# Performance work log

Hardware: AMD Instinct MI355X
Metric: run time of the kernel (lower is better)

The kernel has to match this reference:

```python
import jax, jax.numpy as jnp
import numpy as np

jax.config.update("jax_enable_x64", True)

P = 2013265921          # NTT-friendly prime 15 * 2**27 + 1 (int64-safe proxy for BLS12-377 Fr)
GEN = 31                # generator of the multiplicative group of F_P
LOGN = 22
N = 1 << LOGN           # domain_size
C = 4                   # columns, as in the module docstring example


def _pow_table(base, n):
    """powers[k] = base**k mod P for k in [0, n), built by repeated doubling (vectorized)."""
    pw = np.ones(n, dtype=np.int64)
    cur = base % P
    step = 1
    while step < n:
        hi = min(2 * step, n)
        pw[step:hi] = (pw[:hi - step] * cur) % P
        cur = (cur * cur) % P
        step *= 2
    return pw


def setup_inputs() -> dict:
    key = jax.random.key(0)
    x = jax.random.randint(key, (N, C), 0, P, dtype=jnp.int64)
    omega = pow(GEN, (P - 1) // N, P)          # primitive N-th root of unity
    omega_inv = pow(omega, P - 2, P)           # its inverse (Fermat)
    twiddles = jnp.asarray(_pow_table(omega_inv, N // 2))  # omega_inv**k, k < N/2  (the 'Params' table)
    n_inv = jnp.asarray(pow(N, P - 2, P), dtype=jnp.int64)  # N^{-1} mod P
    return {"input": x, "twiddles": twiddles, "n_inv": n_inv}


def reference(input, twiddles, n_inv):
    """Inverse NTT over F_P, columns transformed independently. Output in natural order."""
    n, c = input.shape
    logn = n.bit_length() - 1
    # bit-reversal permutation indices (static; computed with numpy)
    idx = np.arange(n)
    rev = np.zeros(n, dtype=np.int64)
    for i in range(logn):
        rev = (rev << 1) | ((idx >> i) & 1)
    x = input[rev]
    # iterative Cooley-Tukey butterflies, logn stages
    for s in range(1, logn + 1):
        m = 1 << s
        half = m >> 1
        w = twiddles[:: n // m]                 # [half] = omega_inv**(j * n/m)
        xr = x.reshape(-1, m, c)                # [n/m, m, c]
        lo, hi = xr[:, :half], xr[:, half:]
        t = (w[None, :, None] * hi) % P         # modular twiddle multiply
        x = jnp.concatenate([(lo + t) % P, (lo - t) % P], axis=1).reshape(n, c)
    return (x * n_inv) % P                      # scale by N^{-1}
```

## Files before the change

### kernel.cpp

```cpp
#include <hip/hip_runtime.h>
#include <stdint.h>

static constexpr uint32_t P = 2013265921u;
static constexpr int      LOGM = 11;
static constexpr int      MSZ  = 1 << LOGM;
static constexpr int      NCOL = 2;

__host__ __device__ constexpr uint32_t neg_pinv32() {
    uint32_t x = 1u;
    for (int i = 0; i < 5; ++i) x *= 2u - P * x;
    return 0u - x;
}
static constexpr uint32_t NEG_PINV = neg_pinv32();
static constexpr uint32_t R1 = (uint32_t)(((uint64_t)1 << 32) % P);
static constexpr uint32_t R2 = (uint32_t)(((uint64_t)R1 * R1) % P);

__device__ __forceinline__ uint32_t mont_mul(uint32_t a, uint32_t b) {
    uint32_t tlo = a * b;
    uint32_t thi = __umulhi(a, b);
    uint32_t m   = tlo * NEG_PINV;
    uint32_t r   = thi + __umulhi(m, P) + (tlo != 0u);
    uint32_t s   = r - P;
    return s < r ? s : r;
}
__device__ __forceinline__ uint32_t to_mont(uint32_t a) { return mont_mul(a, R2); }

__device__ __forceinline__ uint32_t shoup_mul(uint32_t w, uint32_t wp, uint32_t x) {
    uint32_t q = __umulhi(wp, x);
    uint32_t t = w * x - q * P;
    uint32_t s = t - P;
    return s < t ? s : t;
}
__device__ __forceinline__ uint32_t add_p(uint32_t a, uint32_t b) {
    uint32_t r = a + b, s = r - P; return s < r ? s : r;
}
__device__ __forceinline__ uint32_t sub_p(uint32_t a, uint32_t b) {
    uint32_t r = a - b, s = r + P; return s < r ? s : r;
}
__device__ __forceinline__ uint4 mm4(uint32_t w, uint4 v) {
    return make_uint4(mont_mul(w, v.x), mont_mul(w, v.y),
                      mont_mul(w, v.z), mont_mul(w, v.w));
}
__device__ __forceinline__ void bf4_sh(uint4& L, uint4& H, uint2 w) {
    uint4 t = make_uint4(shoup_mul(w.x, w.y, H.x), shoup_mul(w.x, w.y, H.y),
                         shoup_mul(w.x, w.y, H.z), shoup_mul(w.x, w.y, H.w));
    uint4 l = L;
    L = make_uint4(add_p(l.x, t.x), add_p(l.y, t.y), add_p(l.z, t.z), add_p(l.w, t.w));
    H = make_uint4(sub_p(l.x, t.x), sub_p(l.y, t.y), sub_p(l.z, t.z), sub_p(l.w, t.w));
}
__device__ __forceinline__ void bf4_mont(uint4& L, uint4& H, uint32_t wm) {
    uint4 t = mm4(wm, H);
    uint4 l = L;
    L = make_uint4(add_p(l.x, t.x), add_p(l.y, t.y), add_p(l.z, t.z), add_p(l.w, t.w));
    H = make_uint4(sub_p(l.x, t.x), sub_p(l.y, t.y), sub_p(l.z, t.z), sub_p(l.w, t.w));
}
__device__ __forceinline__ void bf4_triv(uint4& L, uint4& H) {
    uint4 l = L, h = H;
    L = make_uint4(add_p(l.x, h.x), add_p(l.y, h.y), add_p(l.z, h.z), add_p(l.w, h.w));
    H = make_uint4(sub_p(l.x, h.x), sub_p(l.y, h.y), sub_p(l.z, h.z), sub_p(l.w, h.w));
}

__device__ __forceinline__ int g_sw(int el) {
    return el ^ (((el >> 3) ^ (el >> 6)) & 7);
}
__device__ __forceinline__ int fidx(int el, int c4) { return (g_sw(el) << 1) | c4; }

__device__ __forceinline__ void radix8_sh(uint4 x[8],
        uint2 ta, uint2 tb0, uint2 tb1,
        uint2 tc0, uint2 tc1, uint2 tc2, uint2 tc3) {
    bf4_sh(x[0], x[1], ta);  bf4_sh(x[2], x[3], ta);
    bf4_sh(x[4], x[5], ta);  bf4_sh(x[6], x[7], ta);
    bf4_sh(x[0], x[2], tb0); bf4_sh(x[1], x[3], tb1);
    bf4_sh(x[4], x[6], tb0); bf4_sh(x[5], x[7], tb1);
    bf4_sh(x[0], x[4], tc0); bf4_sh(x[1], x[5], tc1);
    bf4_sh(x[2], x[6], tc2); bf4_sh(x[3], x[7], tc3);
}

template <bool PASS2>
__global__ __launch_bounds__(512, 4) void intt_pass(
        const uint4* __restrict__ src, uint4* __restrict__ dst,
        const uint32_t* __restrict__ tw,
        const uint32_t* __restrict__ ninv_p)
{
    __shared__ uint4 buf[MSZ * NCOL];
    __shared__ uint2 stab[2047];

    const int      t   = threadIdx.x;
    const int      c4  = t & 1;
    const int      sub = t >> 1;
    const uint32_t bid = blockIdx.x;
    const uint32_t grp = ((bid & 7u) << 7) | (bid >> 3);
    const uint32_t c   = (grp << 1) | (uint32_t)c4;

    uint32_t wv[4]; int ev[4];
#pragma unroll
    for (int q = 0; q < 4; ++q) {
        int e = t + (q << 9);
        ev[q] = e;
        if (e < 2047) {
            uint32_t ep1 = (uint32_t)e + 1u;
            int sm1 = 31 - __clz((int)ep1);
            uint32_t j = ep1 - (1u << sm1);
            wv[q] = tw[j << (21 - sm1)];
        }
    }

    const uint32_t r8 = __brev((uint32_t)sub) >> 24;
    uint4 x[8];
#pragma unroll
    for (int m = 0; m < 8; ++m) {
        uint32_t r3 = __brev((uint32_t)m) >> 29;
        x[m] = src[((r3 << 8) | r8) * (uint32_t)MSZ + c];
    }

#pragma unroll
    for (int q = 0; q < 4; ++q) {
        if (ev[q] < 2047) {
            uint32_t w  = wv[q];
            uint32_t wp = (uint32_t)((((uint64_t)w) << 32) / P);
            stab[ev[q]] = make_uint2(w, wp);
        }
    }

    const uint32_t u1 = to_mont(tw[1u << 20]);
    const uint32_t u2 = to_mont(tw[1u << 19]);
    const uint32_t u3 = to_mont(tw[3u << 19]);

    bf4_triv(x[0], x[1]);  bf4_triv(x[2], x[3]);
    bf4_triv(x[4], x[5]);  bf4_triv(x[6], x[7]);
    bf4_triv(x[0], x[2]);  bf4_mont(x[1], x[3], u1);
    bf4_triv(x[4], x[6]);  bf4_mont(x[5], x[7], u1);
    bf4_triv(x[0], x[4]);  bf4_mont(x[1], x[5], u2);
    bf4_mont(x[2], x[6], u1); bf4_mont(x[3], x[7], u3);
#pragma unroll
    for (int m = 0; m < 8; ++m) buf[fidx(8 * sub + m, c4)] = x[m];
    __syncthreads();

    {
        const int L = sub & 7, hi = sub >> 3;
        const int base = (hi << 6) | L;
#pragma unroll
        for (int m = 0; m < 8; ++m) x[m] = buf[fidx(base | (m << 3), c4)];
        radix8_sh(x, stab[7 + L], stab[15 + L], stab[23 + L],
                     stab[31 + L], stab[39 + L], stab[47 + L], stab[55 + L]);
#pragma unroll
        for (int m = 0; m < 8; ++m) buf[fidx(base | (m << 3), c4)] = x[m];
    }
    __syncthreads();

    {
        const int L = sub & 63, hi = sub >> 6;
        const int base = (hi << 9) | L;
#pragma unroll
        for (int m = 0; m < 8; ++m) x[m] = buf[fidx(base | (m << 6), c4)];
        radix8_sh(x, stab[63 + L], stab[127 + L], stab[191 + L],
                     stab[255 + L], stab[319 + L], stab[383 + L], stab[447 + L]);
#pragma unroll
        for (int m = 0; m < 8; ++m) buf[fidx(base | (m << 6), c4)] = x[m];
    }
    __syncthreads();

    uint32_t nm = 0u, s256 = 0u, step512 = 0u, tm0 = 0u;
    if (PASS2) {
        nm = to_mont(*ninv_p);
    } else {
        s256    = to_mont(tw[c << 8]);
        step512 = mont_mul(s256, s256);
        tm0     = to_mont(tw[c * (uint32_t)sub]);
    }
#pragma unroll
    for (int gg = 0; gg < 2; ++gg) {
        const int lo = sub + (gg << 8);
        uint4 y[4];
#pragma unroll
        for (int m = 0; m < 4; ++m) y[m] = buf[fidx(lo | (m << 9), c4)];
        const uint2 t10  = stab[511 + lo];
        const uint2 t110 = stab[1023 + lo];
        const uint2 t111 = stab[1535 + lo];
        bf4_sh(y[0], y[1], t10);  bf4_sh(y[2], y[3], t10);
        bf4_sh(y[0], y[2], t110); bf4_sh(y[1], y[3], t111);

        if (!PASS2) {
            uint32_t tm = tm0;
#pragma unroll
            for (int m = 0; m < 4; ++m) {
                dst[c * (uint32_t)MSZ + (uint32_t)((m << 9) | lo)] = mm4(tm, y[m]);
                tm = mont_mul(tm, step512);
            }
            tm0 = mont_mul(tm0, s256);
        } else {
#pragma unroll
            for (int m = 0; m < 4; ++m)
                dst[(uint32_t)((m << 9) | lo) * (uint32_t)MSZ + c] = mm4(nm, y[m]);
        }
    }
}

extern "C" void kernel_launch(void* const* d_in, const int* in_sizes, int n_in,
                              void* d_out, int out_size, void* d_ws, size_t ws_size,
                              hipStream_t stream)
{
    const uint4*    x    = (const uint4*)d_in[0];
    const uint32_t* tw   = (const uint32_t*)d_in[1];
    const uint32_t* ninv = (const uint32_t*)d_in[2];
    uint4*          out  = (uint4*)d_out;

    intt_pass<false><<<dim3(1024), dim3(512), 0, stream>>>(x, out, tw, ninv);
    intt_pass<true ><<<dim3(1024), dim3(512), 0, stream>>>(out, out, tw, ninv);
}
```

Before: 193.0 us.

## Process two column groups per block with prefetch and shrink twiddle table

Each block now handles two column groups in sequence, halving the grid. While the first group finishes its final stages, the block prefetches the second group's inputs into registers. The Shoup twiddle table is cut from 2047 to 511 entries. The last two stages instead take their twiddles from a 512-entry Montgomery table and derive the remaining ones with extra multiplies. This reduces per-block setup cost (twiddle loads and 64-bit divisions) and overlaps global loads with compute, at the cost of more registers, fewer blocks and extra Montgomery multiplies.

```diff
diff --git a/kernel.cpp b/kernel.cpp
--- a/kernel.cpp
+++ b/kernel.cpp
@@ -82,116 +82,129 @@
         const uint32_t* __restrict__ tw,
         const uint32_t* __restrict__ ninv_p)
 {
-    __shared__ uint4 buf[MSZ * NCOL];
-    __shared__ uint2 stab[2047];
+    __shared__ uint4    buf[MSZ * NCOL];
+    __shared__ uint2    stab[511];
+    __shared__ uint32_t mtab[512];
 
     const int      t   = threadIdx.x;
     const int      c4  = t & 1;
     const int      sub = t >> 1;
     const uint32_t bid = blockIdx.x;
-    const uint32_t grp = ((bid & 7u) << 7) | (bid >> 3);
-    const uint32_t c   = (grp << 1) | (uint32_t)c4;
-
-    uint32_t wv[4]; int ev[4];
-#pragma unroll
-    for (int q = 0; q < 4; ++q) {
-        int e = t + (q << 9);
-        ev[q] = e;
-        if (e < 2047) {
-            uint32_t ep1 = (uint32_t)e + 1u;
-            int sm1 = 31 - __clz((int)ep1);
-            uint32_t j = ep1 - (1u << sm1);
-            wv[q] = tw[j << (21 - sm1)];
-        }
-    }
+    const uint32_t grp = ((bid & 7u) << 6) | (bid >> 3);
+    const uint32_t c0  = (grp << 1) | (uint32_t)c4;
+
+    uint32_t wv = 0u;
+    if (t < 511) {
+        uint32_t ep1 = (uint32_t)t + 1u;
+        int sm1 = 31 - __clz((int)ep1);
+        uint32_t j = ep1 - (1u << sm1);
+        wv = tw[j << (21 - sm1)];
+    }
+    uint32_t mv = tw[(uint32_t)t << 11];
 
     const uint32_t r8 = __brev((uint32_t)sub) >> 24;
     uint4 x[8];
 #pragma unroll
     for (int m = 0; m < 8; ++m) {
         uint32_t r3 = __brev((uint32_t)m) >> 29;
-        x[m] = src[((r3 << 8) | r8) * (uint32_t)MSZ + c];
-    }
-
-#pragma unroll
-    for (int q = 0; q < 4; ++q) {
-        if (ev[q] < 2047) {
-            uint32_t w  = wv[q];
-            uint32_t wp = (uint32_t)((((uint64_t)w) << 32) / P);
-            stab[ev[q]] = make_uint2(w, wp);
-        }
-    }
+        x[m] = src[((r3 << 8) | r8) * (uint32_t)MSZ + c0];
+    }
+
+    if (t < 511) {
+        uint32_t wp = (uint32_t)((((uint64_t)wv) << 32) / P);
+        stab[t] = make_uint2(wv, wp);
+    }
+    mtab[t] = to_mont(mv);
 
     const uint32_t u1 = to_mont(tw[1u << 20]);
     const uint32_t u2 = to_mont(tw[1u << 19]);
     const uint32_t u3 = to_mont(tw[3u << 19]);
-
-    bf4_triv(x[0], x[1]);  bf4_triv(x[2], x[3]);
-    bf4_triv(x[4], x[5]);  bf4_triv(x[6], x[7]);
-    bf4_triv(x[0], x[2]);  bf4_mont(x[1], x[3], u1);
-    bf4_triv(x[4], x[6]);  bf4_mont(x[5], x[7], u1);
-    bf4_triv(x[0], x[4]);  bf4_mont(x[1], x[5], u2);
-    bf4_mont(x[2], x[6], u1); bf4_mont(x[3], x[7], u3);
-#pragma unroll
-    for (int m = 0; m < 8; ++m) buf[fidx(8 * sub + m, c4)] = x[m];
-    __syncthreads();
-
-    {
-        const int L = sub & 7, hi = sub >> 3;
-        const int base = (hi << 6) | L;
-#pragma unroll
-        for (int m = 0; m < 8; ++m) x[m] = buf[fidx(base | (m << 3), c4)];
-        radix8_sh(x, stab[7 + L], stab[15 + L], stab[23 + L],
-                     stab[31 + L], stab[39 + L], stab[47 + L], stab[55 + L]);
-#pragma unroll
-        for (int m = 0; m < 8; ++m) buf[fidx(base | (m << 3), c4)] = x[m];
-    }
-    __syncthreads();
-
-    {
-        const int L = sub & 63, hi = sub >> 6;
-        const int base = (hi << 9) | L;
-#pragma unroll
-        for (int m = 0; m < 8; ++m) x[m] = buf[fidx(base | (m << 6), c4)];
-        radix8_sh(x, stab[63 + L], stab[127 + L], stab[191 + L],
-                     stab[255 + L], stab[319 + L], stab[383 + L], stab[447 + L]);
-#pragma unroll
-        for (int m = 0; m < 8; ++m) buf[fidx(base | (m << 6), c4)] = x[m];
-    }
-    __syncthreads();
-
-    uint32_t nm = 0u, s256 = 0u, step512 = 0u, tm0 = 0u;
-    if (PASS2) {
-        nm = to_mont(*ninv_p);
-    } else {
-        s256    = to_mont(tw[c << 8]);
-        step512 = mont_mul(s256, s256);
-        tm0     = to_mont(tw[c * (uint32_t)sub]);
-    }
-#pragma unroll
-    for (int gg = 0; gg < 2; ++gg) {
-        const int lo = sub + (gg << 8);
-        uint4 y[4];
-#pragma unroll
-        for (int m = 0; m < 4; ++m) y[m] = buf[fidx(lo | (m << 9), c4)];
-        const uint2 t10  = stab[511 + lo];
-        const uint2 t110 = stab[1023 + lo];
-        const uint2 t111 = stab[1535 + lo];
-        bf4_sh(y[0], y[1], t10);  bf4_sh(y[2], y[3], t10);
-        bf4_sh(y[0], y[2], t110); bf4_sh(y[1], y[3], t111);
-
+    uint32_t nm = 0u;
+    if (PASS2) nm = to_mont(*ninv_p);
+
+    uint4 xn[8];
+#pragma unroll
+    for (int it = 0; it < 2; ++it) {
+        const uint32_t c = c0 + (uint32_t)(it << 10);
+        if (it) {
+            __syncthreads();
+#pragma unroll
+            for (int m = 0; m < 8; ++m) x[m] = xn[m];
+        }
+
+        bf4_triv(x[0], x[1]);  bf4_triv(x[2], x[3]);
+        bf4_triv(x[4], x[5]);  bf4_triv(x[6], x[7]);
+        bf4_triv(x[0], x[2]);  bf4_mont(x[1], x[3], u1);
+        bf4_triv(x[4], x[6]);  bf4_mont(x[5], x[7], u1);
+        bf4_triv(x[0], x[4]);  bf4_mont(x[1], x[5], u2);
+        bf4_mont(x[2], x[6], u1); bf4_mont(x[3], x[7], u3);
+#pragma unroll
+        for (int m = 0; m < 8; ++m) buf[fidx(8 * sub + m, c4)] = x[m];
+        __syncthreads();
+
+        {
+            const int L = sub & 7, hi = sub >> 3;
+            const int base = (hi << 6) | L;
+#pragma unroll
+            for (int m = 0; m < 8; ++m) x[m] = buf[fidx(base | (m << 3), c4)];
+            radix8_sh(x, stab[7 + L], stab[15 + L], stab[23 + L],
+                         stab[31 + L], stab[39 + L], stab[47 + L], stab[55 + L]);
+#pragma unroll
+            for (int m = 0; m < 8; ++m) buf[fidx(base | (m << 3), c4)] = x[m];
+        }
+        __syncthreads();
+
+        {
+            const int L = sub & 63, hi = sub >> 6;
+            const int base = (hi << 9) | L;
+#pragma unroll
+            for (int m = 0; m < 8; ++m) x[m] = buf[fidx(base | (m << 6), c4)];
+            radix8_sh(x, stab[63 + L], stab[127 + L], stab[191 + L],
+                         stab[255 + L], stab[319 + L], stab[383 + L], stab[447 + L]);
+#pragma unroll
+            for (int m = 0; m < 8; ++m) buf[fidx(base | (m << 6), c4)] = x[m];
+        }
+        __syncthreads();
+
+        if (it == 0) {
+#pragma unroll
+            for (int m = 0; m < 8; ++m) {
+                uint32_t r3 = __brev((uint32_t)m) >> 29;
+                xn[m] = src[((r3 << 8) | r8) * (uint32_t)MSZ + (c0 + 1024u)];
+            }
+        }
+
+        uint32_t s256 = 0u, step512 = 0u, tm0 = 0u;
         if (!PASS2) {
-            uint32_t tm = tm0;
-#pragma unroll
-            for (int m = 0; m < 4; ++m) {
-                dst[c * (uint32_t)MSZ + (uint32_t)((m << 9) | lo)] = mm4(tm, y[m]);
-                tm = mont_mul(tm, step512);
+            s256    = to_mont(tw[c << 8]);
+            step512 = mont_mul(s256, s256);
+            tm0     = to_mont(tw[c * (uint32_t)sub]);
+        }
+#pragma unroll
+        for (int gg = 0; gg < 2; ++gg) {
+            const int lo = sub + (gg << 8);
+            uint4 y[4];
+#pragma unroll
+            for (int m = 0; m < 4; ++m) y[m] = buf[fidx(lo | (m << 9), c4)];
+            const uint32_t M    = mtab[lo];
+            const uint32_t t10  = mont_mul(M, M);
+            const uint32_t t111 = mont_mul(M, u1);
+            bf4_mont(y[0], y[1], t10);  bf4_mont(y[2], y[3], t10);
+            bf4_mont(y[0], y[2], M);    bf4_mont(y[1], y[3], t111);
+
+            if (!PASS2) {
+                uint32_t tm = tm0;
+#pragma unroll
+                for (int m = 0; m < 4; ++m) {
+                    dst[c * (uint32_t)MSZ + (uint32_t)((m << 9) | lo)] = mm4(tm, y[m]);
+                    tm = mont_mul(tm, step512);
+                }
+                tm0 = mont_mul(tm0, s256);
+            } else {
+#pragma unroll
+                for (int m = 0; m < 4; ++m)
+                    dst[(uint32_t)((m << 9) | lo) * (uint32_t)MSZ + c] = mm4(nm, y[m]);
             }
-            tm0 = mont_mul(tm0, s256);
-        } else {
-#pragma unroll
-            for (int m = 0; m < 4; ++m)
-                dst[(uint32_t)((m << 9) | lo) * (uint32_t)MSZ + c] = mm4(nm, y[m]);
         }
     }
 }
@@ -205,6 +218,6 @@
     const uint32_t* ninv = (const uint32_t*)d_in[2];
     uint4*          out  = (uint4*)d_out;
 
-    intt_pass<false><<<dim3(1024), dim3(512), 0, stream>>>(x, out, tw, ninv);
-    intt_pass<true ><<<dim3(1024), dim3(512), 0, stream>>>(out, out, tw, ninv);
-}
+    intt_pass<false><<<dim3(512), dim3(512), 0, stream>>>(x, out, tw, ninv);
+    intt_pass<true ><<<dim3(512), dim3(512), 0, stream>>>(out, out, tw, ninv);
+}
```

New measurement: 205.4 us. +6.4%, slower.

## Restructure per-block 2048-point NTT as radix-16/16/8 with 256 threads

Applied to the files above, without the earlier changes.

Replaces the radix-8/8/8/4 decomposition over 512 threads with radix-16, radix-16, then radix-8 stages over 256 threads, each holding 16 elements in registers. This cuts the number of shared-memory round trips and barriers per pass. The shared twiddle table shrinks to 255 Shoup entries plus a 256-entry Montgomery table, and the last-stage twiddles are computed on the fly from products. The bank swizzle changes to match the new access strides. The cost is higher register pressure per thread, lower occupancy (launch bounds 256,2) and extra Montgomery multiplies in the final stage.

```diff
diff --git a/kernel.cpp b/kernel.cpp
--- a/kernel.cpp
+++ b/kernel.cpp
@@ -4,7 +4,6 @@
 static constexpr uint32_t P = 2013265921u;
 static constexpr int      LOGM = 11;
 static constexpr int      MSZ  = 1 << LOGM;
-static constexpr int      NCOL = 2;
 
 __host__ __device__ constexpr uint32_t neg_pinv32() {
     uint32_t x = 1u;
@@ -61,29 +60,19 @@
 }
 
 __device__ __forceinline__ int g_sw(int el) {
-    return el ^ (((el >> 3) ^ (el >> 6)) & 7);
+    return el ^ (((el >> 4) ^ (el >> 8)) & 3);
 }
 __device__ __forceinline__ int fidx(int el, int c4) { return (g_sw(el) << 1) | c4; }
 
-__device__ __forceinline__ void radix8_sh(uint4 x[8],
-        uint2 ta, uint2 tb0, uint2 tb1,
-        uint2 tc0, uint2 tc1, uint2 tc2, uint2 tc3) {
-    bf4_sh(x[0], x[1], ta);  bf4_sh(x[2], x[3], ta);
-    bf4_sh(x[4], x[5], ta);  bf4_sh(x[6], x[7], ta);
-    bf4_sh(x[0], x[2], tb0); bf4_sh(x[1], x[3], tb1);
-    bf4_sh(x[4], x[6], tb0); bf4_sh(x[5], x[7], tb1);
-    bf4_sh(x[0], x[4], tc0); bf4_sh(x[1], x[5], tc1);
-    bf4_sh(x[2], x[6], tc2); bf4_sh(x[3], x[7], tc3);
-}
-
 template <bool PASS2>
-__global__ __launch_bounds__(512, 4) void intt_pass(
+__global__ __launch_bounds__(256, 2) void intt_pass(
         const uint4* __restrict__ src, uint4* __restrict__ dst,
         const uint32_t* __restrict__ tw,
         const uint32_t* __restrict__ ninv_p)
 {
-    __shared__ uint4 buf[MSZ * NCOL];
-    __shared__ uint2 stab[2047];
+    __shared__ uint4    buf[MSZ * 2];
+    __shared__ uint2    stab[255];
+    __shared__ uint32_t mtab[256];
 
     const int      t   = threadIdx.x;
     const int      c4  = t & 1;
@@ -92,106 +81,135 @@
     const uint32_t grp = ((bid & 7u) << 7) | (bid >> 3);
     const uint32_t c   = (grp << 1) | (uint32_t)c4;
 
-    uint32_t wv[4]; int ev[4];
-#pragma unroll
-    for (int q = 0; q < 4; ++q) {
-        int e = t + (q << 9);
-        ev[q] = e;
-        if (e < 2047) {
-            uint32_t ep1 = (uint32_t)e + 1u;
-            int sm1 = 31 - __clz((int)ep1);
-            uint32_t j = ep1 - (1u << sm1);
-            wv[q] = tw[j << (21 - sm1)];
-        }
-    }
-
-    const uint32_t r8 = __brev((uint32_t)sub) >> 24;
-    uint4 x[8];
-#pragma unroll
-    for (int m = 0; m < 8; ++m) {
-        uint32_t r3 = __brev((uint32_t)m) >> 29;
-        x[m] = src[((r3 << 8) | r8) * (uint32_t)MSZ + c];
-    }
-
-#pragma unroll
-    for (int q = 0; q < 4; ++q) {
-        if (ev[q] < 2047) {
-            uint32_t w  = wv[q];
-            uint32_t wp = (uint32_t)((((uint64_t)w) << 32) / P);
-            stab[ev[q]] = make_uint2(w, wp);
-        }
-    }
+    uint32_t wv = 0u;
+    const bool hasst = (t >= 15) && (t < 255);
+    if (hasst) {
+        uint32_t ep1 = (uint32_t)t + 1u;
+        int sm1 = 31 - __clz((int)ep1);
+        uint32_t j = ep1 - (1u << sm1);
+        wv = tw[j << (21 - sm1)];
+    }
+    uint32_t mv = tw[(uint32_t)t << 11];
+
+    const uint32_t r7 = __brev((uint32_t)sub) >> 25;
+    uint4 x[16];
+#pragma unroll
+    for (int i = 0; i < 16; ++i) {
+        const uint32_t r4 = __brev((uint32_t)i) >> 28;
+        x[i] = src[((r4 << 7) | r7) * (uint32_t)MSZ + c];
+    }
+
+    if (hasst) {
+        uint32_t wp = (uint32_t)((((uint64_t)wv) << 32) / P);
+        stab[t] = make_uint2(wv, wp);
+    }
+    mtab[t] = to_mont(mv);
 
     const uint32_t u1 = to_mont(tw[1u << 20]);
     const uint32_t u2 = to_mont(tw[1u << 19]);
     const uint32_t u3 = to_mont(tw[3u << 19]);
-
-    bf4_triv(x[0], x[1]);  bf4_triv(x[2], x[3]);
-    bf4_triv(x[4], x[5]);  bf4_triv(x[6], x[7]);
-    bf4_triv(x[0], x[2]);  bf4_mont(x[1], x[3], u1);
-    bf4_triv(x[4], x[6]);  bf4_mont(x[5], x[7], u1);
-    bf4_triv(x[0], x[4]);  bf4_mont(x[1], x[5], u2);
-    bf4_mont(x[2], x[6], u1); bf4_mont(x[3], x[7], u3);
-#pragma unroll
-    for (int m = 0; m < 8; ++m) buf[fidx(8 * sub + m, c4)] = x[m];
+    uint32_t v4[8];
+    v4[0] = 0u;
+#pragma unroll
+    for (int j = 1; j < 8; ++j) v4[j] = to_mont(tw[(uint32_t)j << 18]);
+
+#pragma unroll
+    for (int p = 0; p < 8; ++p) bf4_triv(x[2 * p], x[2 * p + 1]);
+#pragma unroll
+    for (int q = 0; q < 4; ++q) {
+        bf4_triv(x[4 * q],     x[4 * q + 2]);
+        bf4_mont(x[4 * q + 1], x[4 * q + 3], u1);
+    }
+#pragma unroll
+    for (int h = 0; h < 2; ++h) {
+        const int b = 8 * h;
+        bf4_triv(x[b],     x[b + 4]);
+        bf4_mont(x[b + 1], x[b + 5], u2);
+        bf4_mont(x[b + 2], x[b + 6], u1);
+        bf4_mont(x[b + 3], x[b + 7], u3);
+    }
+    bf4_triv(x[0], x[8]);
+#pragma unroll
+    for (int i = 1; i < 8; ++i) bf4_mont(x[i], x[i + 8], v4[i]);
+
+#pragma unroll
+    for (int i = 0; i < 16; ++i) buf[fidx(16 * sub + i, c4)] = x[i];
+
     __syncthreads();
 
-    {
-        const int L = sub & 7, hi = sub >> 3;
-        const int base = (hi << 6) | L;
-#pragma unroll
-        for (int m = 0; m < 8; ++m) x[m] = buf[fidx(base | (m << 3), c4)];
-        radix8_sh(x, stab[7 + L], stab[15 + L], stab[23 + L],
-                     stab[31 + L], stab[39 + L], stab[47 + L], stab[55 + L]);
-#pragma unroll
-        for (int m = 0; m < 8; ++m) buf[fidx(base | (m << 3), c4)] = x[m];
-    }
+    const int lo4 = sub >> 3;
+    const int k   = sub & 7;
+#pragma unroll
+    for (int m = 0; m < 16; ++m) x[m] = buf[fidx(k * 256 + m * 16 + lo4, c4)];
+
+    const uint2 T5    = stab[15 + lo4];
+    const uint2 T6a   = stab[31 + lo4],  T6b = stab[47 + lo4];
+    uint2 T7[4];
+#pragma unroll
+    for (int r = 0; r < 4; ++r) T7[r] = stab[63 + 16 * r + lo4];
+    uint2 T8[8];
+#pragma unroll
+    for (int r = 0; r < 8; ++r) T8[r] = stab[127 + 16 * r + lo4];
+
+#pragma unroll
+    for (int p = 0; p < 8; ++p) bf4_sh(x[2 * p], x[2 * p + 1], T5);
+#pragma unroll
+    for (int q = 0; q < 4; ++q) {
+        bf4_sh(x[4 * q],     x[4 * q + 2], T6a);
+        bf4_sh(x[4 * q + 1], x[4 * q + 3], T6b);
+    }
+#pragma unroll
+    for (int h = 0; h < 2; ++h) {
+#pragma unroll
+        for (int r = 0; r < 4; ++r) bf4_sh(x[8 * h + r], x[8 * h + r + 4], T7[r]);
+    }
+#pragma unroll
+    for (int r = 0; r < 8; ++r) bf4_sh(x[r], x[r + 8], T8[r]);
+
+#pragma unroll
+    for (int m = 0; m < 16; ++m) buf[fidx(k * 256 + m * 16 + lo4, c4)] = x[m];
+
     __syncthreads();
 
-    {
-        const int L = sub & 63, hi = sub >> 6;
-        const int base = (hi << 9) | L;
-#pragma unroll
-        for (int m = 0; m < 8; ++m) x[m] = buf[fidx(base | (m << 6), c4)];
-        radix8_sh(x, stab[63 + L], stab[127 + L], stab[191 + L],
-                     stab[255 + L], stab[319 + L], stab[383 + L], stab[447 + L]);
-#pragma unroll
-        for (int m = 0; m < 8; ++m) buf[fidx(base | (m << 6), c4)] = x[m];
-    }
-    __syncthreads();
-
-    uint32_t nm = 0u, s256 = 0u, step512 = 0u, tm0 = 0u;
-    if (PASS2) {
-        nm = to_mont(*ninv_p);
-    } else {
-        s256    = to_mont(tw[c << 8]);
-        step512 = mont_mul(s256, s256);
-        tm0     = to_mont(tw[c * (uint32_t)sub]);
-    }
-#pragma unroll
-    for (int gg = 0; gg < 2; ++gg) {
-        const int lo = sub + (gg << 8);
-        uint4 y[4];
-#pragma unroll
-        for (int m = 0; m < 4; ++m) y[m] = buf[fidx(lo | (m << 9), c4)];
-        const uint2 t10  = stab[511 + lo];
-        const uint2 t110 = stab[1023 + lo];
-        const uint2 t111 = stab[1535 + lo];
-        bf4_sh(y[0], y[1], t10);  bf4_sh(y[2], y[3], t10);
-        bf4_sh(y[0], y[2], t110); bf4_sh(y[1], y[3], t111);
+    const int la = 32 * k + lo4;
+    const int lb = la + 16;
+    uint32_t s256 = 0u, nm = 0u;
+    if (PASS2) nm = to_mont(*ninv_p);
+    else       s256 = to_mont(tw[c << 8]);
+
+#pragma unroll
+    for (int g = 0; g < 2; ++g) {
+        const int r = g ? lb : la;
+        uint4 y[8];
+#pragma unroll
+        for (int m = 0; m < 8; ++m) y[m] = buf[fidx(m * 256 + r, c4)];
+
+        const uint32_t M    = mtab[r];
+        const uint32_t M2   = mont_mul(M, M);
+        const uint32_t t9   = mont_mul(M2, M2);
+        const uint32_t t10b = mont_mul(M2, u1);
+        const uint32_t t111 = mont_mul(M, u2);
+        const uint32_t t112 = mont_mul(M, u1);
+        const uint32_t t113 = mont_mul(M, u3);
+
+        bf4_mont(y[0], y[1], t9); bf4_mont(y[2], y[3], t9);
+        bf4_mont(y[4], y[5], t9); bf4_mont(y[6], y[7], t9);
+        bf4_mont(y[0], y[2], M2);   bf4_mont(y[1], y[3], t10b);
+        bf4_mont(y[4], y[6], M2);   bf4_mont(y[5], y[7], t10b);
+        bf4_mont(y[0], y[4], M);    bf4_mont(y[1], y[5], t111);
+        bf4_mont(y[2], y[6], t112); bf4_mont(y[3], y[7], t113);
 
         if (!PASS2) {
-            uint32_t tm = tm0;
-#pragma unroll
-            for (int m = 0; m < 4; ++m) {
-                dst[c * (uint32_t)MSZ + (uint32_t)((m << 9) | lo)] = mm4(tm, y[m]);
-                tm = mont_mul(tm, step512);
+            uint32_t tm = to_mont(tw[c * (uint32_t)r]);
+#pragma unroll
+            for (int m = 0; m < 8; ++m) {
+                dst[c * (uint32_t)MSZ + (uint32_t)(m * 256 + r)] = mm4(tm, y[m]);
+                tm = mont_mul(tm, s256);
             }
-            tm0 = mont_mul(tm0, s256);
         } else {
 #pragma unroll
-            for (int m = 0; m < 4; ++m)
-                dst[(uint32_t)((m << 9) | lo) * (uint32_t)MSZ + c] = mm4(nm, y[m]);
+            for (int m = 0; m < 8; ++m)
+                dst[(uint32_t)(m * 256 + r) * (uint32_t)MSZ + c] = mm4(nm, y[m]);
         }
     }
 }
@@ -205,6 +223,6 @@
     const uint32_t* ninv = (const uint32_t*)d_in[2];
     uint4*          out  = (uint4*)d_out;
 
-    intt_pass<false><<<dim3(1024), dim3(512), 0, stream>>>(x, out, tw, ninv);
-    intt_pass<true ><<<dim3(1024), dim3(512), 0, stream>>>(out, out, tw, ninv);
-}
+    intt_pass<false><<<dim3(1024), dim3(256), 0, stream>>>(x, out, tw, ninv);
+    intt_pass<true ><<<dim3(1024), dim3(256), 0, stream>>>(out, out, tw, ninv);
+}
```

Measured after the change: 202.3 us. 4.9% more time.
